# Performance work log

Measured on AMD Instinct MI355X. Metric: run time of the kernel, lower is better.

The kernel has to match this reference:

```python
import jax, jax.numpy as jnp
import numpy as np

NEG_SLOPE = 0.2
EPS = 1e-16

def gat_layer(x, W, a_src, a_dst, bias, src, dst, N, H, C):
    # x: [N, F_in]; W: [F_in, H*C]; a_src/a_dst: [H, C]; bias: [H*C]
    h = (x @ W).reshape(N, H, C)                       # [N,H,C]
    alpha_src = (h * a_src[None]).sum(-1)              # [N,H]
    alpha_dst = (h * a_dst[None]).sum(-1)              # [N,H]
    e = jax.nn.leaky_relu(alpha_src[src] + alpha_dst[dst], NEG_SLOPE)  # [E,H]
    m = jax.ops.segment_max(e, dst, num_segments=N)    # [N,H]
    ex = jnp.exp(e - m[dst])
    s = jax.ops.segment_sum(ex, dst, num_segments=N)   # [N,H]
    alpha = ex / (s[dst] + EPS)                        # [E,H]
    out = jax.ops.segment_sum(h[src] * alpha[:, :, None], dst, num_segments=N)  # [N,H,C]
    return out.reshape(N, H * C) + bias

def setup_inputs() -> dict:
    key = jax.random.key(0)
    ks = jax.random.split(key, 12)
    N, E, Ep = 50000, 800000, 100000
    Fin, Hd, Co, H = 128, 128, 64, 2
    x = jax.random.normal(ks[0], (N, Fin), jnp.float32)
    edge_index = jax.random.randint(ks[1], (2, E), 0, N, jnp.int64)
    pos_edge_index = jax.random.randint(ks[2], (2, Ep), 0, N, jnp.int64)
    W1 = jax.random.normal(ks[3], (Fin, H * Hd), jnp.float32) / np.sqrt(Fin)
    a1_src = jax.random.normal(ks[4], (H, Hd), jnp.float32) / np.sqrt(Hd)
    a1_dst = jax.random.normal(ks[5], (H, Hd), jnp.float32) / np.sqrt(Hd)
    b1 = jnp.zeros((H * Hd,), jnp.float32)
    W2 = jax.random.normal(ks[6], (H * Hd, H * Co), jnp.float32) / np.sqrt(H * Hd)
    a2_src = jax.random.normal(ks[7], (H, Co), jnp.float32) / np.sqrt(Co)
    a2_dst = jax.random.normal(ks[8], (H, Co), jnp.float32) / np.sqrt(Co)
    b2 = jnp.zeros((H * Co,), jnp.float32)
    return {"x": x, "edge_index": edge_index, "pos_edge_index": pos_edge_index,
            "W1": W1, "a1_src": a1_src, "a1_dst": a1_dst, "b1": b1,
            "W2": W2, "a2_src": a2_src, "a2_dst": a2_dst, "b2": b2}

def reference(x, edge_index, pos_edge_index, W1, a1_src, a1_dst, b1, W2, a2_src, a2_dst, b2):
    N = x.shape[0]
    H = a1_src.shape[0]
    # add self loops (PyG GATConv default)
    loop = jnp.arange(N, dtype=edge_index.dtype)
    src = jnp.concatenate([edge_index[0], loop])
    dst = jnp.concatenate([edge_index[1], loop])
    h1 = gat_layer(x, W1, a1_src, a1_dst, b1, src, dst, N, H, a1_src.shape[1])
    h1 = jax.nn.relu(h1)  # dropout is identity in eval mode
    z = gat_layer(h1, W2, a2_src, a2_dst, b2, src, dst, N, H, a2_src.shape[1])
    # decode: dot product per positive edge
    return (z[pos_edge_index[0]] * z[pos_edge_index[1]]).sum(-1)
```

## Files before the change

### kernel.cpp

```cpp
#include <hip/hip_runtime.h>

#define NEG_SLOPE 0.2f
#define EPS_F 1e-16f
#define STILE 4096

typedef short short8 __attribute__((ext_vector_type(8)));
typedef float f32x4 __attribute__((ext_vector_type(4)));

__device__ __forceinline__ unsigned short f2bf(float x) {
    unsigned u = __float_as_uint(x);
    return (unsigned short)((u + 0x7FFFu + ((u >> 16) & 1u)) >> 16);
}
__device__ __forceinline__ float bflo(unsigned q) { return __uint_as_float(q << 16); }
__device__ __forceinline__ float bfhi(unsigned q) { return __uint_as_float(q & 0xFFFF0000u); }


template<int MB, int K, typename TIN>
__device__ __forceinline__ void gemm_body(
        const TIN* __restrict__ X, const unsigned short* __restrict__ Wt,
        unsigned short* __restrict__ Y, float* __restrict__ as_out,
        float* __restrict__ ad_out, const float* __restrict__ a_srcf,
        const float* __restrict__ a_dstf, int N, int bid,
        unsigned short* lds) {
    constexpr int NT_ = MB / 16;
    constexpr int C   = MB / 2;
    constexpr int KS  = K / 32;
    constexpr int KP  = K + 8;
    int tid  = threadIdx.x;
    int w    = tid >> 6, lane = tid & 63;
    int li   = lane & 15, kc = lane >> 4;
    int n0   = bid * 64 + w * 16;
    int arow = min(n0 + li, N - 1);

    constexpr int CHUNKS = MB * K / 8;
#pragma unroll
    for (int c = 0; c < CHUNKS / 256; ++c) {
        int id = tid + c * 256;
        int m = id / (K / 8), k8 = id % (K / 8);
        *(uint4*)&lds[m * KP + k8 * 8] = *(const uint4*)&Wt[m * K + k8 * 8];
    }
    short8 a[KS];
#pragma unroll
    for (int ks = 0; ks < KS; ++ks) {
        if constexpr (sizeof(TIN) == 4) {
            const float* xp = (const float*)X + (size_t)arow * K + ks * 32 + kc * 8;
            float4 xa = *(const float4*)xp;
            float4 xb = *(const float4*)(xp + 4);
            a[ks][0] = (short)f2bf(xa.x); a[ks][1] = (short)f2bf(xa.y);
            a[ks][2] = (short)f2bf(xa.z); a[ks][3] = (short)f2bf(xa.w);
            a[ks][4] = (short)f2bf(xb.x); a[ks][5] = (short)f2bf(xb.y);
            a[ks][6] = (short)f2bf(xb.z); a[ks][7] = (short)f2bf(xb.w);
        } else {
            a[ks] = *(const short8*)((const unsigned short*)X + (size_t)arow * K + ks * 32 + kc * 8);
        }
    }
    __syncthreads();

    f32x4 acc[NT_];
#pragma unroll
    for (int ct = 0; ct < NT_; ++ct) acc[ct] = (f32x4){0.f, 0.f, 0.f, 0.f};
#pragma unroll
    for (int ct = 0; ct < NT_; ++ct) {
        const unsigned short* wb = lds + (ct * 16 + li) * KP + kc * 8;
#pragma unroll
        for (int ks = 0; ks < KS; ++ks) {
            short8 b = *(const short8*)(wb + ks * 32);
            acc[ct] = __builtin_amdgcn_mfma_f32_16x16x32_bf16(a[ks], b, acc[ct], 0, 0, 0);
        }
    }

    float av[NT_], dv[NT_];
#pragma unroll
    for (int ct = 0; ct < NT_; ++ct) {
        av[ct] = a_srcf[ct * 16 + li];
        dv[ct] = a_dstf[ct * 16 + li];
    }
    int row_base = n0 + kc * 4;
#pragma unroll
    for (int r = 0; r < 4; ++r) {
        int n = row_base + r;
        float vs0 = 0.f, vs1 = 0.f, vd0 = 0.f, vd1 = 0.f;
#pragma unroll
        for (int ct = 0; ct < NT_; ++ct) {
            float v = acc[ct][r];
            if (ct * 16 < C) { vs0 = fmaf(v, av[ct], vs0); vd0 = fmaf(v, dv[ct], vd0); }
            else             { vs1 = fmaf(v, av[ct], vs1); vd1 = fmaf(v, dv[ct], vd1); }
        }
#pragma unroll
        for (int off = 1; off < 16; off <<= 1) {
            vs0 += __shfl_xor(vs0, off);
            vs1 += __shfl_xor(vs1, off);
            vd0 += __shfl_xor(vd0, off);
            vd1 += __shfl_xor(vd1, off);
        }
        if (n < N) {
            if (li == 0) {
                as_out[n * 2] = vs0; as_out[n * 2 + 1] = vs1;
                ad_out[n * 2] = vd0; ad_out[n * 2 + 1] = vd1;
            }
#pragma unroll
            for (int ct = 0; ct < NT_; ++ct)
                Y[(size_t)n * MB + ct * 16 + li] = f2bf(acc[ct][r]);
        }
    }
}

__device__ __forceinline__ void scan_part_body(const int* __restrict__ deg,
                                               int* __restrict__ tsum, int b) {
    __shared__ int wsh[4];
    int t = threadIdx.x;
    int base = b * STILE + t * 16;
    int sum = 0;
#pragma unroll
    for (int j = 0; j < 16; j += 4) {
        int4 q = *(const int4*)&deg[base + j];
        sum += q.x + q.y + q.z + q.w;
    }
#pragma unroll
    for (int off = 32; off; off >>= 1) sum += __shfl_down(sum, off);
    if ((t & 63) == 0) wsh[t >> 6] = sum;
    __syncthreads();
    if (t == 0) tsum[b] = wsh[0] + wsh[1] + wsh[2] + wsh[3];
}

__device__ __forceinline__ void fill_body(const int* __restrict__ ei, int E, int N,
                                          const int* __restrict__ rowptr,
                                          int* __restrict__ cursor,
                                          int* __restrict__ csr_src, int bid) {
    int e = bid * 256 + threadIdx.x;
    if (e >= E + N) return;
    int s, d;
    if (e < E) { s = ei[e]; d = ei[E + e]; } else { s = d = e - E; }
    int pos = atomicAdd(&cursor[d], 1);
    csr_src[rowptr[d] + pos] = s;
}


__global__ void k_prep_hist(const float* __restrict__ W1, unsigned short* __restrict__ Wt1,
                            int K1, int M1,
                            const float* __restrict__ W2, unsigned short* __restrict__ Wt2,
                            int K2, int M2, int nPrepBlk,
                            const int* __restrict__ ei, int E, int N,
                            int* __restrict__ deg) {
    if ((int)blockIdx.x < nPrepBlk) {
        int i = blockIdx.x * 256 + threadIdx.x;
        int n1 = M1 * K1;
        if (i < n1) {
            int m = i / K1, k = i - m * K1;
            Wt1[i] = f2bf(W1[(size_t)k * M1 + m]);
        } else {
            int j = i - n1;
            if (j < M2 * K2) {
                int m = j / K2, k = j - m * K2;
                Wt2[j] = f2bf(W2[(size_t)k * M2 + m]);
            }
        }
    } else {
        int e = (blockIdx.x - nPrepBlk) * 256 + threadIdx.x;
        if (e >= E + N) return;
        int d = (e < E) ? ei[E + e] : e - E;
        atomicAdd(&deg[d], 1);
    }
}

__global__ __launch_bounds__(256) void k_scan_part(const int* __restrict__ deg,
                                                   int* __restrict__ tsum) {
    scan_part_body(deg, tsum, blockIdx.x);
}

__global__ __launch_bounds__(256) void scan_final(const int* __restrict__ deg,
                                                  const int* __restrict__ tsum,
                                                  int* __restrict__ rowptr,
                                                  int* __restrict__ cursor) {
    int b = blockIdx.x, t = threadIdx.x, lane = t & 63, wid = t >> 6;
    int base = b * STILE + t * 16;
    int tpre = 0;
    for (int j = 0; j < b; ++j) tpre += tsum[j];
    int v[16];
    int sum = 0;
#pragma unroll
    for (int j = 0; j < 16; j += 4) {
        int4 q = *(const int4*)&deg[base + j];
        v[j] = q.x; v[j + 1] = q.y; v[j + 2] = q.z; v[j + 3] = q.w;
        sum += q.x + q.y + q.z + q.w;
    }
    int x = sum;
#pragma unroll
    for (int off = 1; off < 64; off <<= 1) {
        int y = __shfl_up(x, off);
        if (lane >= off) x += y;
    }
    __shared__ int wtot[4];
    if (lane == 63) wtot[wid] = x;
    __syncthreads();
    int woff = 0;
    for (int wi = 0; wi < wid; ++wi) woff += wtot[wi];
    int run = tpre + woff + (x - sum);
    int outv[16];
#pragma unroll
    for (int j = 0; j < 16; ++j) { outv[j] = run; run += v[j]; }
#pragma unroll
    for (int j = 0; j < 16; j += 4) {
        *(int4*)&rowptr[base + j] = make_int4(outv[j], outv[j+1], outv[j+2], outv[j+3]);
        *(int4*)&cursor[base + j] = make_int4(0, 0, 0, 0);
    }
}

__global__ __launch_bounds__(256) void k_gemm1_fill(
        const float* __restrict__ X, const unsigned short* __restrict__ Wt,
        unsigned short* __restrict__ Y, float* __restrict__ as_out,
        float* __restrict__ ad_out, const float* __restrict__ a_srcf,
        const float* __restrict__ a_dstf, int N, int GB,
        const int* __restrict__ ei, int E,
        const int* __restrict__ rowptr, int* __restrict__ cursor,
        int* __restrict__ csr_src) {
    __shared__ __align__(16) unsigned short lds[256 * (128 + 8)];
    if ((int)blockIdx.x < GB)
        gemm_body<256, 128, float>(X, Wt, Y, as_out, ad_out, a_srcf, a_dstf, N,
                                   blockIdx.x, lds);
    else
        fill_body(ei, E, N, rowptr, cursor, csr_src, blockIdx.x - GB);
}

__global__ __launch_bounds__(256) void k_gemm2(
        const unsigned short* __restrict__ X, const unsigned short* __restrict__ Wt,
        unsigned short* __restrict__ Y, float* __restrict__ as_out,
        float* __restrict__ ad_out, const float* __restrict__ a_srcf,
        const float* __restrict__ a_dstf, int N) {
    __shared__ __align__(16) unsigned short lds[128 * (256 + 8)];
    gemm_body<128, 256, unsigned short>(X, Wt, Y, as_out, ad_out, a_srcf, a_dstf, N,
                                        blockIdx.x, lds);
}

template<int M, int C, typename TOUT>
__global__ __launch_bounds__(256) void fused_attn_agg(
        const int* __restrict__ rowptr, const int* __restrict__ csr_src,
        const float* __restrict__ as_, const float* __restrict__ ad_,
        const unsigned short* __restrict__ hfeat, const float* __restrict__ bias,
        TOUT* __restrict__ outp, int N, int do_relu) {
    constexpr int VEC = M / 64;
    __shared__ __align__(16) uint2 pb0[4][64];
    __shared__ __align__(16) uint2 pb1[4][64];
    int n    = (blockIdx.x * blockDim.x + threadIdx.x) >> 6;
    int lane = threadIdx.x & 63;
    int w    = (threadIdx.x >> 6) & 3;
    if (n >= N) return;
    int cbase = lane * VEC;
    int hh    = cbase / C;
    int r0 = rowptr[n], r1 = rowptr[n + 1];
    const float2* as2 = (const float2*)as_;
    float2 adv = ((const float2*)ad_)[n];
    float sa0 = 0.f, sa1 = 0.f;
    float acc[VEC];
#pragma unroll
    for (int v = 0; v < VEC; ++v) acc[v] = 0.f;
    const uint2* ap = (hh == 0) ? pb0[w] : pb1[w];
    const char* hbc = (const char*)hfeat + (size_t)cbase * 2;

    for (int base = r0; base < r1; base += 64) {
        int cnt = min(64, r1 - base);
        int srcl = 0;
        float sc0 = -INFINITY, sc1 = -INFINITY;
        if (lane < cnt) {
            srcl = csr_src[base + lane];
            float2 asv = as2[srcl];
            float e0 = asv.x + adv.x;
            float e1 = asv.y + adv.y;
            sc0 = (e0 > 0.f) ? e0 : NEG_SLOPE * e0;
            sc1 = (e1 > 0.f) ? e1 : NEG_SLOPE * e1;
        }
        float p0 = expf(sc0), p1 = expf(sc1);
        sa0 += p0; sa1 += p1;
        unsigned off = (unsigned)srcl * (M * 2);
        pb0[w][lane] = make_uint2(off, __float_as_uint(p0));
        pb1[w][lane] = make_uint2(off, __float_as_uint(p1));
        for (int e = 0; e < cnt; e += 2) {
            uint4 qq = *(const uint4*)&ap[e];
            float pa = __uint_as_float(qq.y);
            float pc = __uint_as_float(qq.w);
            const char* hp0 = hbc + qq.x;
            const char* hp1 = hbc + qq.z;
            if constexpr (VEC == 4) {
                uint2 g0 = *(const uint2*)hp0;
                uint2 g1 = *(const uint2*)hp1;
                acc[0] += pa * bflo(g0.x); acc[1] += pa * bfhi(g0.x);
                acc[2] += pa * bflo(g0.y); acc[3] += pa * bfhi(g0.y);
                acc[0] += pc * bflo(g1.x); acc[1] += pc * bfhi(g1.x);
                acc[2] += pc * bflo(g1.y); acc[3] += pc * bfhi(g1.y);
            } else {
                unsigned g0 = *(const unsigned*)hp0;
                unsigned g1 = *(const unsigned*)hp1;
                acc[0] += pa * bflo(g0); acc[1] += pa * bfhi(g0);
                acc[0] += pc * bflo(g1); acc[1] += pc * bfhi(g1);
            }
        }
    }
#pragma unroll
    for (int off = 32; off; off >>= 1) {
        sa0 += __shfl_xor(sa0, off);
        sa1 += __shfl_xor(sa1, off);
    }
    float ssum = (hh == 0) ? sa0 : sa1;
    float inv = 1.f / (ssum + EPS_F);
    float o[VEC];
#pragma unroll
    for (int v = 0; v < VEC; ++v) {
        float val = acc[v] * inv + bias[cbase + v];
        o[v] = do_relu ? fmaxf(val, 0.f) : val;
    }
    if constexpr (sizeof(TOUT) == 2) {
        unsigned short* op = (unsigned short*)outp + (size_t)n * M + cbase;
        if constexpr (VEC == 4) {
            uint2 pk;
            pk.x = (unsigned)f2bf(o[0]) | ((unsigned)f2bf(o[1]) << 16);
            pk.y = (unsigned)f2bf(o[2]) | ((unsigned)f2bf(o[3]) << 16);
            *(uint2*)op = pk;
        } else {
            *(unsigned*)op = (unsigned)f2bf(o[0]) | ((unsigned)f2bf(o[1]) << 16);
        }
    } else {
        float* op = (float*)outp + (size_t)n * M + cbase;
        if constexpr (VEC == 4) *(float4*)op = make_float4(o[0], o[1], o[2], o[3]);
        else                    *(float2*)op = make_float2(o[0], o[1]);
    }
}

__global__ void decode_kernel(const int* __restrict__ pei, int Ep,
                              const unsigned short* __restrict__ z, int D,
                              float* __restrict__ out) {
    int wv   = (blockIdx.x * blockDim.x + threadIdx.x) >> 6;
    int lane = threadIdx.x & 63;
    int half = lane >> 5, sl = lane & 31;
    int e  = wv * 2 + half;
    int ec = min(e, Ep - 1);
    int a = pei[ec], b = pei[Ep + ec];
    uint2 qa = *(const uint2*)(z + (size_t)a * D + sl * 4);
    uint2 qb = *(const uint2*)(z + (size_t)b * D + sl * 4);
    float s = bflo(qa.x) * bflo(qb.x) + bfhi(qa.x) * bfhi(qb.x)
            + bflo(qa.y) * bflo(qb.y) + bfhi(qa.y) * bfhi(qb.y);
#pragma unroll
    for (int off = 16; off; off >>= 1) s += __shfl_xor(s, off);
    if (sl == 0 && e < Ep) out[e] = s;
}

extern "C" void kernel_launch(void* const* d_in, const int* in_sizes, int n_in,
                              void* d_out, int out_size, void* d_ws, size_t ws_size,
                              hipStream_t stream) {
    const float* x   = (const float*)d_in[0];
    const int*   ei  = (const int*)d_in[1];
    const int*   pei = (const int*)d_in[2];
    const float* W1  = (const float*)d_in[3];
    const float* a1s = (const float*)d_in[4];
    const float* a1d = (const float*)d_in[5];
    const float* b1  = (const float*)d_in[6];
    const float* W2  = (const float*)d_in[7];
    const float* a2s = (const float*)d_in[8];
    const float* a2d = (const float*)d_in[9];
    const float* b2  = (const float*)d_in[10];
    float* out = (float*)d_out;

    const int M1  = in_sizes[6];
    const int Fin = in_sizes[3] / M1;
    const int N   = in_sizes[0] / Fin;
    const int E   = in_sizes[1] / 2;
    const int Ep  = in_sizes[2] / 2;
    const int M2  = in_sizes[10];
    const int Etot = E + N;
    const int NT  = (N + STILE - 1) / STILE;

    unsigned short* hbf  = (unsigned short*)d_ws;
    unsigned short* h1bf = hbf + (size_t)N * M1;
    unsigned short* zbf  = h1bf + (size_t)N * M1;
    float* as_     = (float*)(zbf + (size_t)N * M2);
    float* ad_     = as_ + (size_t)N * 2;
    int*   deg     = (int*)(ad_ + (size_t)N * 2);
    int*   rowptr  = deg + (size_t)NT * STILE;
    int*   cursor  = rowptr + (size_t)NT * STILE;
    int*   tsum    = cursor + (size_t)NT * STILE;
    int*   csr_src = tsum + 64;
    unsigned short* wt1 = (unsigned short*)(csr_src + Etot);
    unsigned short* wt2 = wt1 + (size_t)M1 * Fin;

    dim3 blk256(256);

    hipMemsetAsync(deg, 0, (size_t)NT * STILE * sizeof(int), stream);

    int nPrepBlk = (M1 * Fin + M2 * M1 + 255) / 256;
    int nHistBlk = (Etot + 255) / 256;
    k_prep_hist<<<nPrepBlk + nHistBlk, blk256, 0, stream>>>(
        W1, wt1, Fin, M1, W2, wt2, M1, M2, nPrepBlk, ei, E, N, deg);

    k_scan_part<<<NT, blk256, 0, stream>>>(deg, tsum);
    scan_final<<<NT, blk256, 0, stream>>>(deg, tsum, rowptr, cursor);

    int GB = (N + 63) / 64;
    k_gemm1_fill<<<GB + nHistBlk, blk256, 0, stream>>>(
        x, wt1, hbf, as_, ad_, a1s, a1d, N, GB,
        ei, E, rowptr, cursor, csr_src);

    fused_attn_agg<256, 128, unsigned short><<<(N + 3) / 4, blk256, 0, stream>>>(
        rowptr, csr_src, as_, ad_, hbf, b1, h1bf, N, 1);

    k_gemm2<<<(N + 63) / 64, blk256, 0, stream>>>(
        h1bf, wt2, hbf, as_, ad_, a2s, a2d, N);

    fused_attn_agg<128, 64, unsigned short><<<(N + 3) / 4, blk256, 0, stream>>>(
        rowptr, csr_src, as_, ad_, hbf, b2, zbf, N, 0);

    {
        int waves = (Ep + 1) / 2;
        decode_kernel<<<(waves * 64 + 255) / 256, blk256, 0, stream>>>(
            pei, Ep, zbf, M2, out);
    }
}
```

Baseline: 239.2 us.

## Record per-edge slot in histogram pass and overlap scan with GEMM1

The histogram pass now stores each edge's atomicAdd return value as its slot within the destination row. This removes the second round of atomics on a cursor array and the need to zero that cursor. The partial scan is merged into the GEMM1 launch, and the CSR fill becomes a separate atomic-free scatter kernel. In exchange it needs an extra per-edge position array, and the fill no longer overlaps with GEMM1.

Measured after the change: 208.4 us. 12.9% less time.

```diff
diff --git a/kernel.cpp b/kernel.cpp
--- a/kernel.cpp
+++ b/kernel.cpp
@@ -123,25 +123,13 @@
     if (t == 0) tsum[b] = wsh[0] + wsh[1] + wsh[2] + wsh[3];
 }
 
-__device__ __forceinline__ void fill_body(const int* __restrict__ ei, int E, int N,
-                                          const int* __restrict__ rowptr,
-                                          int* __restrict__ cursor,
-                                          int* __restrict__ csr_src, int bid) {
-    int e = bid * 256 + threadIdx.x;
-    if (e >= E + N) return;
-    int s, d;
-    if (e < E) { s = ei[e]; d = ei[E + e]; } else { s = d = e - E; }
-    int pos = atomicAdd(&cursor[d], 1);
-    csr_src[rowptr[d] + pos] = s;
-}
-
 
 __global__ void k_prep_hist(const float* __restrict__ W1, unsigned short* __restrict__ Wt1,
                             int K1, int M1,
                             const float* __restrict__ W2, unsigned short* __restrict__ Wt2,
                             int K2, int M2, int nPrepBlk,
                             const int* __restrict__ ei, int E, int N,
-                            int* __restrict__ deg) {
+                            int* __restrict__ deg, int* __restrict__ pos) {
     if ((int)blockIdx.x < nPrepBlk) {
         int i = blockIdx.x * 256 + threadIdx.x;
         int n1 = M1 * K1;
@@ -159,19 +147,27 @@
         int e = (blockIdx.x - nPrepBlk) * 256 + threadIdx.x;
         if (e >= E + N) return;
         int d = (e < E) ? ei[E + e] : e - E;
-        atomicAdd(&deg[d], 1);
-    }
-}
-
-__global__ __launch_bounds__(256) void k_scan_part(const int* __restrict__ deg,
-                                                   int* __restrict__ tsum) {
-    scan_part_body(deg, tsum, blockIdx.x);
+        pos[e] = atomicAdd(&deg[d], 1);
+    }
+}
+
+__global__ __launch_bounds__(256) void k_gemm1_scan(
+        const float* __restrict__ X, const unsigned short* __restrict__ Wt,
+        unsigned short* __restrict__ Y, float* __restrict__ as_out,
+        float* __restrict__ ad_out, const float* __restrict__ a_srcf,
+        const float* __restrict__ a_dstf, int N, int GB,
+        const int* __restrict__ deg, int* __restrict__ tsum) {
+    __shared__ __align__(16) unsigned short lds[256 * (128 + 8)];
+    if ((int)blockIdx.x < GB)
+        gemm_body<256, 128, float>(X, Wt, Y, as_out, ad_out, a_srcf, a_dstf, N,
+                                   blockIdx.x, lds);
+    else
+        scan_part_body(deg, tsum, blockIdx.x - GB);
 }
 
 __global__ __launch_bounds__(256) void scan_final(const int* __restrict__ deg,
                                                   const int* __restrict__ tsum,
-                                                  int* __restrict__ rowptr,
-                                                  int* __restrict__ cursor) {
+                                                  int* __restrict__ rowptr) {
     int b = blockIdx.x, t = threadIdx.x, lane = t & 63, wid = t >> 6;
     int base = b * STILE + t * 16;
     int tpre = 0;
@@ -200,26 +196,18 @@
 #pragma unroll
     for (int j = 0; j < 16; ++j) { outv[j] = run; run += v[j]; }
 #pragma unroll
-    for (int j = 0; j < 16; j += 4) {
+    for (int j = 0; j < 16; j += 4)
         *(int4*)&rowptr[base + j] = make_int4(outv[j], outv[j+1], outv[j+2], outv[j+3]);
-        *(int4*)&cursor[base + j] = make_int4(0, 0, 0, 0);
-    }
-}
-
-__global__ __launch_bounds__(256) void k_gemm1_fill(
-        const float* __restrict__ X, const unsigned short* __restrict__ Wt,
-        unsigned short* __restrict__ Y, float* __restrict__ as_out,
-        float* __restrict__ ad_out, const float* __restrict__ a_srcf,
-        const float* __restrict__ a_dstf, int N, int GB,
-        const int* __restrict__ ei, int E,
-        const int* __restrict__ rowptr, int* __restrict__ cursor,
-        int* __restrict__ csr_src) {
-    __shared__ __align__(16) unsigned short lds[256 * (128 + 8)];
-    if ((int)blockIdx.x < GB)
-        gemm_body<256, 128, float>(X, Wt, Y, as_out, ad_out, a_srcf, a_dstf, N,
-                                   blockIdx.x, lds);
-    else
-        fill_body(ei, E, N, rowptr, cursor, csr_src, blockIdx.x - GB);
+}
+
+__global__ void fill_kernel(const int* __restrict__ ei, int E, int N,
+                            const int* __restrict__ rowptr, const int* __restrict__ pos,
+                            int* __restrict__ csr_src) {
+    int e = blockIdx.x * blockDim.x + threadIdx.x;
+    if (e >= E + N) return;
+    int s, d;
+    if (e < E) { s = ei[e]; d = ei[E + e]; } else { s = d = e - E; }
+    csr_src[rowptr[d] + pos[e]] = s;
 }
 
 __global__ __launch_bounds__(256) void k_gemm2(
@@ -375,9 +363,9 @@
     float* ad_     = as_ + (size_t)N * 2;
     int*   deg     = (int*)(ad_ + (size_t)N * 2);
     int*   rowptr  = deg + (size_t)NT * STILE;
-    int*   cursor  = rowptr + (size_t)NT * STILE;
-    int*   tsum    = cursor + (size_t)NT * STILE;
-    int*   csr_src = tsum + 64;
+    int*   tsum    = rowptr + (size_t)NT * STILE;
+    int*   pos     = tsum + 64;
+    int*   csr_src = pos + Etot;
     unsigned short* wt1 = (unsigned short*)(csr_src + Etot);
     unsigned short* wt2 = wt1 + (size_t)M1 * Fin;
 
@@ -388,15 +376,15 @@
     int nPrepBlk = (M1 * Fin + M2 * M1 + 255) / 256;
     int nHistBlk = (Etot + 255) / 256;
     k_prep_hist<<<nPrepBlk + nHistBlk, blk256, 0, stream>>>(
-        W1, wt1, Fin, M1, W2, wt2, M1, M2, nPrepBlk, ei, E, N, deg);
-
-    k_scan_part<<<NT, blk256, 0, stream>>>(deg, tsum);
-    scan_final<<<NT, blk256, 0, stream>>>(deg, tsum, rowptr, cursor);
+        W1, wt1, Fin, M1, W2, wt2, M1, M2, nPrepBlk, ei, E, N, deg, pos);
 
     int GB = (N + 63) / 64;
-    k_gemm1_fill<<<GB + nHistBlk, blk256, 0, stream>>>(
-        x, wt1, hbf, as_, ad_, a1s, a1d, N, GB,
-        ei, E, rowptr, cursor, csr_src);
+    k_gemm1_scan<<<GB + NT, blk256, 0, stream>>>(
+        x, wt1, hbf, as_, ad_, a1s, a1d, N, GB, deg, tsum);
+
+    scan_final<<<NT, blk256, 0, stream>>>(deg, tsum, rowptr);
+
+    fill_kernel<<<nHistBlk, blk256, 0, stream>>>(ei, E, N, rowptr, pos, csr_src);
 
     fused_attn_agg<256, 128, unsigned short><<<(N + 3) / 4, blk256, 0, stream>>>(
         rowptr, csr_src, as_, ad_, hbf, b1, h1bf, N, 1);
```
